# Optimization experiments

Measured on AMD Instinct MI355X. Metric: run time of the kernel, lower is better.

Reference implementation:

```python
import jax, jax.numpy as jnp
import numpy as np

B, S, D, V, H, P, L, STEPS = 8, 128, 512, 32768, 8, 2048, 4, 3
DK = D // H
SCALE = 1.0 / np.sqrt(DK)


def setup_inputs() -> dict:
    key = jax.random.key(0)
    ks = jax.random.split(key, 16)

    def n(k, shape, s=0.02):
        return jax.random.normal(k, shape, dtype=jnp.float32) * s

    return {
        'tokens': jax.random.randint(ks[0], (B, S), 0, V, dtype=jnp.int32),
        'emb': n(ks[1], (V, D)),
        'in_proj_w': n(ks[2], (L, 3 * D, D)),
        'in_proj_b': jnp.zeros((L, 3 * D), jnp.float32),
        'attn_out_w': n(ks[3], (L, D, D)),
        'attn_out_b': jnp.zeros((L, D), jnp.float32),
        'ln1_w': jnp.ones((L, D), jnp.float32),
        'ln1_b': jnp.zeros((L, D), jnp.float32),
        'lstm_wih': n(ks[4], (L, 4 * D, D)),
        'lstm_whh': n(ks[5], (L, 4 * D, D)),
        'lstm_bih': jnp.zeros((L, 4 * D), jnp.float32),
        'lstm_bhh': jnp.zeros((L, 4 * D), jnp.float32),
        'ff_w1': n(ks[6], (L, P, D)),
        'ff_b1': jnp.zeros((L, P), jnp.float32),
        'ff_w2': n(ks[7], (L, D, P)),
        'ff_b2': jnp.zeros((L, D), jnp.float32),
        'ln2_w': jnp.ones((L, D), jnp.float32),
        'ln2_b': jnp.zeros((L, D), jnp.float32),
        'head_w': n(ks[8], (V, D)),
        'head_b': jnp.zeros((V,), jnp.float32),
    }


def _layernorm(x, w, b, eps=1e-5):
    m = x.mean(-1, keepdims=True)
    v = x.var(-1, keepdims=True)
    return (x - m) * jax.lax.rsqrt(v + eps) * w + b


def _forward(tokens, emb, in_proj_w, in_proj_b, attn_out_w, attn_out_b,
             ln1_w, ln1_b, lstm_wih, lstm_whh, lstm_bih, lstm_bhh,
             ff_w1, ff_b1, ff_w2, ff_b2, ln2_w, ln2_b, head_w, head_b):
    # embedding; PositionalEncoding.forward in the source is a no-op (returns x)
    x = emb[tokens]                       # (B, S, D)
    x = x.transpose(1, 0, 2)              # seq-first (S, B, D) like nn.MultiheadAttention
    causal = jnp.triu(jnp.ones((S, S), bool), 1)  # True above diagonal -> masked

    for l in range(L):
        # --- self attention (eval mode, dropout=0) ---
        qkv = x @ in_proj_w[l].T + in_proj_b[l]        # (S, B, 3D)
        q, k, v = jnp.split(qkv, 3, axis=-1)
        def heads(t):  # (S, B, D) -> (B, H, S, DK)
            return t.reshape(S, B, H, DK).transpose(1, 2, 0, 3)
        q, k, v = heads(q), heads(k), heads(v)
        scores = jnp.einsum('bhqd,bhkd->bhqk', q, k) * SCALE
        scores = jnp.where(causal, jnp.finfo(scores.dtype).min, scores)
        w = jax.nn.softmax(scores, axis=-1)
        o = jnp.einsum('bhqk,bhkd->bhqd', w, v)        # (B, H, S, DK)
        o = o.transpose(2, 0, 1, 3).reshape(S, B, D)
        attn = o @ attn_out_w[l].T + attn_out_b[l]
        x = _layernorm(x + attn, ln1_w[l], ln1_b[l])

        # --- latent recurrence: per-token LSTM cell carried for STEPS steps ---
        residual = x
        latent = x.transpose(1, 0, 2).reshape(B * S, D)  # (B*S, D)
        h = jnp.zeros_like(latent)
        c = jnp.zeros_like(latent)
        for _ in range(STEPS):
            gates = latent @ lstm_wih[l].T + lstm_bih[l] + h @ lstm_whh[l].T + lstm_bhh[l]
            i_g, f_g, g_g, o_g = jnp.split(gates, 4, axis=-1)  # torch gate order i,f,g,o
            c = jax.nn.sigmoid(f_g) * c + jax.nn.sigmoid(i_g) * jnp.tanh(g_g)
            h = jax.nn.sigmoid(o_g) * jnp.tanh(c)
            latent = h
        latent = latent.reshape(B, S, D).transpose(1, 0, 2)  # (S, B, D)
        latent = residual + latent

        # --- feed forward ---
        ff = jax.nn.relu(latent @ ff_w1[l].T + ff_b1[l]) @ ff_w2[l].T + ff_b2[l]
        x = _layernorm(latent + ff, ln2_w[l], ln2_b[l])

    logits = x @ head_w.T + head_b        # (S, B, V)
    return logits.transpose(1, 0, 2)      # (B, S, V)


def reference(tokens, emb, in_proj_w, in_proj_b, attn_out_w, attn_out_b,
              ln1_w, ln1_b, lstm_wih, lstm_whh, lstm_bih, lstm_bhh,
              ff_w1, ff_b1, ff_w2, ff_b2, ln2_w, ln2_b, head_w, head_b):
    return _forward(tokens, emb, in_proj_w, in_proj_b, attn_out_w, attn_out_b,
                    ln1_w, ln1_b, lstm_wih, lstm_whh, lstm_bih, lstm_bhh,
                    ff_w1, ff_b1, ff_w2, ff_b2, ln2_w, ln2_b, head_w, head_b)
```

## Files before the change

kernel.cpp:

```cpp
#include <hip/hip_runtime.h>
#include <hip/hip_bf16.h>
#include <math.h>

typedef unsigned short ushort_t;
typedef __bf16 bf16x8 __attribute__((ext_vector_type(8)));
typedef float f32x4 __attribute__((ext_vector_type(4)));

constexpr int Bb = 8, Ss = 128, Dd = 512, Vv = 32768, Hh = 8, Pp = 2048, Ll = 4;
constexpr int Tt = Bb * Ss;
constexpr int DK = Dd / Hh;
constexpr float SCALE = 0.125f;

__device__ __forceinline__ ushort_t f2b(float f) {
    unsigned u = __float_as_uint(f);
    unsigned r = (u + 0x7FFFu + ((u >> 16) & 1u)) >> 16;
    return (ushort_t)r;
}

__device__ __forceinline__ void gload_lds16(const void* g, void* l) {
    __builtin_amdgcn_global_load_lds((const __attribute__((address_space(1))) void*)g,
                                     (__attribute__((address_space(3))) void*)l, 16, 0, 0);
}

struct CvtSegs {
    const float* a[8];
    const float* b[8];
    void*        d[8];
    long         end4[8];
    int          mode[8];
};

__global__ __launch_bounds__(256) void cvt_all_k(CvtSegs s) {
    long i = (long)blockIdx.x * 256 + threadIdx.x;
    int k = 0;
    while (k < 7 && i >= s.end4[k]) ++k;
    long base = k ? s.end4[k - 1] : 0;
    long j = i - base;
    int mode = s.mode[k];
    long srcj = j;
    if (mode == 2 || mode == 3) {
        const long per = 2048L * 128;
        long layer = j / per, rem = j % per;
        long drow = rem >> 7, col4 = rem & 127;
        long g = (drow >> 4) & 3, d = (drow >> 6) * 16 + (drow & 15);
        srcj = layer * per + (g * 512 + d) * 128 + col4;
    } else if (mode == 4) {
        const long per = 512;
        long layer = j / per, rem = j % per;
        long e0 = rem * 4;
        long g = (e0 >> 4) & 3, d = (e0 >> 6) * 16 + (e0 & 15);
        srcj = layer * per + (g * 512 + d) / 4;
    }
    float4 v = reinterpret_cast<const float4*>(s.a[k])[srcj];
    if (s.b[k]) {
        float4 vb = reinterpret_cast<const float4*>(s.b[k])[srcj];
        v.x += vb.x; v.y += vb.y; v.z += vb.z; v.w += vb.w;
    }
    if (mode == 4) {
        reinterpret_cast<float4*>(s.d[k])[j] = v;
    } else {
        ushort4 o;
        o.x = f2b(v.x); o.y = f2b(v.y); o.z = f2b(v.z); o.w = f2b(v.w);
        reinterpret_cast<ushort4*>(s.d[k])[j] = o;
    }
}

__global__ __launch_bounds__(128) void embed_k(const int* __restrict__ tokens,
                                               const float* __restrict__ emb,
                                               float* __restrict__ X,
                                               ushort_t* __restrict__ Xb) {
    int t = blockIdx.x;
    int tok = tokens[t];
    float4 v = reinterpret_cast<const float4*>(emb + (long)tok * Dd)[threadIdx.x];
    reinterpret_cast<float4*>(X + (long)t * Dd)[threadIdx.x] = v;
    ushort4 o;
    o.x = f2b(v.x); o.y = f2b(v.y); o.z = f2b(v.z); o.w = f2b(v.w);
    reinterpret_cast<ushort4*>(Xb + (long)t * Dd)[threadIdx.x] = o;
}

template <int BM, int BN, int BK, int EPI>
__global__ __launch_bounds__(256) void gemm_bf16(const ushort_t* __restrict__ A,
                                                 const ushort_t* __restrict__ W,
                                                 const float* __restrict__ b1,
                                                 float* __restrict__ C,
                                                 ushort_t* __restrict__ Cb,
                                                 float* __restrict__ cst,
                                                 const float* __restrict__ addsrc,
                                                 float* __restrict__ lat,
                                                 ushort_t* __restrict__ latb,
                                                 int M, int N, int K) {
    constexpr int CH = BK / 8;
    constexpr int SH = (CH == 4) ? 1 : 0;
    constexpr int WM = BM / 2, WN = BN / 2;
    constexpr int FM = WM / 16, FN = WN / 16;
    constexpr int LA = BM * BK / 2048;
    constexpr int LW = BN * BK / 2048;

    __shared__ __align__(16) ushort_t As[2][BM * BK];
    __shared__ __align__(16) ushort_t Ws[2][BN * BK];

    const int tid = threadIdx.x;
    const int lane = tid & 63, wid = tid >> 6;
    const int wr = wid >> 1, wc = wid & 1;
    const int row0 = blockIdx.y * BM, col0 = blockIdx.x * BN;

    auto stage = [&](int buf, int k0) {
#pragma unroll
        for (int i = 0; i < LA; ++i) {
            int j = i * 256 + tid;
            int prow = j / CH;
            int pkg = j & (CH - 1);
            int skg = pkg ^ ((prow >> SH) & (CH - 1));
            gload_lds16(A + (long)(row0 + prow) * K + k0 + skg * 8,
                        &As[buf][(i * 256 + wid * 64) * 8]);
        }
#pragma unroll
        for (int i = 0; i < LW; ++i) {
            int j = i * 256 + tid;
            int prow = j / CH;
            int pkg = j & (CH - 1);
            int skg = pkg ^ ((prow >> SH) & (CH - 1));
            gload_lds16(W + (long)(col0 + prow) * K + k0 + skg * 8,
                        &Ws[buf][(i * 256 + wid * 64) * 8]);
        }
    };

    f32x4 acc[FM][FN];
#pragma unroll
    for (int m = 0; m < FM; ++m)
#pragma unroll
        for (int n = 0; n < FN; ++n) acc[m][n] = (f32x4)(0.0f);

    const int NT = K / BK;
    stage(0, 0);
    __syncthreads();
    for (int t = 0; t < NT; ++t) {
        int cur = t & 1;
        if (t + 1 < NT) stage(cur ^ 1, (t + 1) * BK);
        const ushort_t* Ab = As[cur];
        const ushort_t* Wb = Ws[cur];
#pragma unroll
        for (int kk = 0; kk < BK / 32; ++kk) {
            bf16x8 af[FM], wf[FN];
#pragma unroll
            for (int m = 0; m < FM; ++m) {
                int r = wr * WM + m * 16 + (lane & 15);
                int cl = kk * 4 + (lane >> 4);
                int cs = cl ^ ((r >> SH) & (CH - 1));
                af[m] = *reinterpret_cast<const bf16x8*>(&Ab[r * BK + cs * 8]);
            }
#pragma unroll
            for (int n = 0; n < FN; ++n) {
                int r = wc * WN + n * 16 + (lane & 15);
                int cl = kk * 4 + (lane >> 4);
                int cs = cl ^ ((r >> SH) & (CH - 1));
                wf[n] = *reinterpret_cast<const bf16x8*>(&Wb[r * BK + cs * 8]);
            }
#pragma unroll
            for (int m = 0; m < FM; ++m)
#pragma unroll
                for (int n = 0; n < FN; ++n)
                    acc[m][n] = __builtin_amdgcn_mfma_f32_16x16x32_bf16(
                        af[m], wf[n], acc[m][n], 0, 0, 0);
        }
        __syncthreads();
    }

    if constexpr (EPI <= 2) {
#pragma unroll
        for (int n = 0; n < FN; ++n) {
            int col = col0 + wc * WN + n * 16 + (lane & 15);
            float bias = b1[col];
#pragma unroll
            for (int m = 0; m < FM; ++m) {
#pragma unroll
                for (int j = 0; j < 4; ++j) {
                    int row = row0 + wr * WM + m * 16 + (lane >> 4) * 4 + j;
                    float v = acc[m][n][j] + bias;
                    if (EPI == 2) v = fmaxf(v, 0.f);
                    if (EPI == 0) C[(long)row * N + col] = v;
                    else          Cb[(long)row * N + col] = f2b(v);
                }
            }
        }
    } else {
        const int L = lane & 15;
        const int d = ((col0 >> 6) + wc) * 16 + L;
        float bI = b1[col0 + wc * WN + 0 * 16 + L];
        float bF = b1[col0 + wc * WN + 1 * 16 + L];
        float bG = b1[col0 + wc * WN + 2 * 16 + L];
        float bO = b1[col0 + wc * WN + 3 * 16 + L];
#pragma unroll
        for (int m = 0; m < FM; ++m) {
#pragma unroll
            for (int j = 0; j < 4; ++j) {
                int row = row0 + wr * WM + m * 16 + (lane >> 4) * 4 + j;
                long idx = (long)row * Dd + d;
                float gi = acc[m][0][j] + bI;
                float gf = acc[m][1][j] + bF;
                float gg = acc[m][2][j] + bG;
                float go = acc[m][3][j] + bO;
                float si = 1.f / (1.f + expf(-gi));
                float sf = 1.f / (1.f + expf(-gf));
                float so = 1.f / (1.f + expf(-go));
                float cold = (EPI == 3) ? 0.f : cst[idx];
                float cn = sf * cold + si * tanhf(gg);
                float hn = so * tanhf(cn);
                if (EPI == 5) {
                    float o = addsrc[idx] + hn;
                    lat[idx] = o;
                    latb[idx] = f2b(o);
                } else {
                    cst[idx] = cn;
                    Cb[idx] = f2b(hn);
                }
            }
        }
    }
}

__global__ __launch_bounds__(256) void attn_k(const ushort_t* __restrict__ qkv,
                                              ushort_t* __restrict__ Ob) {
    const int blk = blockIdx.x;
    const int qb = blk & 1;
    const int bh = blk >> 1;
    const int h = bh & 7, b = bh >> 3;
    const int tid = threadIdx.x, lane = tid & 63, wid = tid >> 6;
    const int wr = wid >> 1, wc = wid & 1;
    const long qp = 3 * Dd;

    __shared__ __align__(16) char smem[32768];
    ushort_t* Qs = (ushort_t*)smem;
    ushort_t* Ks = (ushort_t*)(smem + 8192);
    float*    Sf = (float*)smem;
    ushort_t* Ps = (ushort_t*)smem;
    ushort_t* Vt = (ushort_t*)(smem + 16384);

#pragma unroll
    for (int i = 0; i < 2; ++i) {
        int j = i * 256 + tid;
        int r = j >> 3, cl = j & 7, cs = cl ^ (r & 7);
        bf16x8 v = *reinterpret_cast<const bf16x8*>(
            qkv + (long)(b * Ss + qb * 64 + r) * qp + h * DK + cl * 8);
        *reinterpret_cast<bf16x8*>(Qs + r * 64 + cs * 8) = v;
    }
#pragma unroll
    for (int i = 0; i < 4; ++i) {
        int j = i * 256 + tid;
        int r = j >> 3, cl = j & 7, cs = cl ^ (r & 7);
        bf16x8 v = *reinterpret_cast<const bf16x8*>(
            qkv + (long)(b * Ss + r) * qp + Dd + h * DK + cl * 8);
        *reinterpret_cast<bf16x8*>(Ks + r * 64 + cs * 8) = v;
    }
    __syncthreads();

    f32x4 acc[2][4];
#pragma unroll
    for (int m = 0; m < 2; ++m)
#pragma unroll
        for (int n = 0; n < 4; ++n) acc[m][n] = (f32x4)(0.0f);
#pragma unroll
    for (int kk = 0; kk < 2; ++kk) {
        bf16x8 af[2], wf[4];
#pragma unroll
        for (int m = 0; m < 2; ++m) {
            int r = wr * 32 + m * 16 + (lane & 15);
            int cl = kk * 4 + (lane >> 4), cs = cl ^ (r & 7);
            af[m] = *reinterpret_cast<const bf16x8*>(Qs + r * 64 + cs * 8);
        }
#pragma unroll
        for (int n = 0; n < 4; ++n) {
            int r = wc * 64 + n * 16 + (lane & 15);
            int cl = kk * 4 + (lane >> 4), cs = cl ^ (r & 7);
            wf[n] = *reinterpret_cast<const bf16x8*>(Ks + r * 64 + cs * 8);
        }
#pragma unroll
        for (int m = 0; m < 2; ++m)
#pragma unroll
            for (int n = 0; n < 4; ++n)
                acc[m][n] = __builtin_amdgcn_mfma_f32_16x16x32_bf16(
                    af[m], wf[n], acc[m][n], 0, 0, 0);
    }
    __syncthreads();
#pragma unroll
    for (int m = 0; m < 2; ++m)
#pragma unroll
        for (int n = 0; n < 4; ++n)
#pragma unroll
            for (int j = 0; j < 4; ++j) {
                int row = wr * 32 + m * 16 + (lane >> 4) * 4 + j;
                int col = wc * 64 + n * 16 + (lane & 15);
                Sf[row * 128 + col] = acc[m][n][j] * SCALE;
            }
    __syncthreads();

    const int r = tid >> 2, q4 = tid & 3;
    const int qglob = qb * 64 + r;
    const int kbase = q4 * 32;
    float pv[32];
    float mx = -INFINITY;
#pragma unroll
    for (int i4 = 0; i4 < 8; ++i4) {
        int c4 = (i4 + (r & 7)) & 7;
        float4 v = *reinterpret_cast<const float4*>(&Sf[r * 128 + kbase + c4 * 4]);
#pragma unroll
        for (int e = 0; e < 4; ++e) {
            int kcol = kbase + c4 * 4 + e;
            float s = (e == 0) ? v.x : (e == 1) ? v.y : (e == 2) ? v.z : v.w;
            pv[i4 * 4 + e] = s;
            if (kcol <= qglob) mx = fmaxf(mx, s);
        }
    }
    mx = fmaxf(mx, __shfl_xor(mx, 1));
    mx = fmaxf(mx, __shfl_xor(mx, 2));
    float sum = 0.f;
#pragma unroll
    for (int i4 = 0; i4 < 8; ++i4) {
        int c4 = (i4 + (r & 7)) & 7;
#pragma unroll
        for (int e = 0; e < 4; ++e) {
            int kcol = kbase + c4 * 4 + e;
            float p = (kcol <= qglob) ? expf(pv[i4 * 4 + e] - mx) : 0.f;
            pv[i4 * 4 + e] = p;
            sum += p;
        }
    }
    sum += __shfl_xor(sum, 1);
    sum += __shfl_xor(sum, 2);
    float inv = 1.f / sum;
    __syncthreads();

#pragma unroll
    for (int i4 = 0; i4 < 8; ++i4) {
        int c4 = (i4 + (r & 7)) & 7;
#pragma unroll
        for (int e2 = 0; e2 < 2; ++e2) {
            int k0 = kbase + c4 * 4 + e2 * 2;
            int cl = k0 >> 3, cs = cl ^ (r & 15);
            ushort2 pr;
            pr.x = f2b(pv[i4 * 4 + e2 * 2] * inv);
            pr.y = f2b(pv[i4 * 4 + e2 * 2 + 1] * inv);
            *reinterpret_cast<ushort2*>(Ps + r * 128 + cs * 8 + (k0 & 7)) = pr;
        }
    }
#pragma unroll
    for (int i = 0; i < 4; ++i) {
        int j = i * 256 + tid;
        int s = j >> 3, dc = j & 7;
        bf16x8 v = *reinterpret_cast<const bf16x8*>(
            qkv + (long)(b * Ss + s) * qp + 2 * Dd + h * DK + dc * 8);
        int cl = s >> 3;
#pragma unroll
        for (int e = 0; e < 8; ++e) {
            int d = dc * 8 + e;
            int cs = cl ^ (d & 15);
            Vt[d * 128 + cs * 8 + (s & 7)] = ((ushort_t*)&v)[e];
        }
    }
    __syncthreads();

    f32x4 acc2[2][2];
#pragma unroll
    for (int m = 0; m < 2; ++m)
#pragma unroll
        for (int n = 0; n < 2; ++n) acc2[m][n] = (f32x4)(0.0f);
#pragma unroll
    for (int kk = 0; kk < 4; ++kk) {
        bf16x8 af[2], wf[2];
#pragma unroll
        for (int m = 0; m < 2; ++m) {
            int rr = wr * 32 + m * 16 + (lane & 15);
            int cl = kk * 4 + (lane >> 4), cs = cl ^ (rr & 15);
            af[m] = *reinterpret_cast<const bf16x8*>(Ps + rr * 128 + cs * 8);
        }
#pragma unroll
        for (int n = 0; n < 2; ++n) {
            int rd = wc * 32 + n * 16 + (lane & 15);
            int cl = kk * 4 + (lane >> 4), cs = cl ^ (rd & 15);
            wf[n] = *reinterpret_cast<const bf16x8*>(Vt + rd * 128 + cs * 8);
        }
#pragma unroll
        for (int m = 0; m < 2; ++m)
#pragma unroll
            for (int n = 0; n < 2; ++n)
                acc2[m][n] = __builtin_amdgcn_mfma_f32_16x16x32_bf16(
                    af[m], wf[n], acc2[m][n], 0, 0, 0);
    }
#pragma unroll
    for (int m = 0; m < 2; ++m)
#pragma unroll
        for (int n = 0; n < 2; ++n)
#pragma unroll
            for (int j = 0; j < 4; ++j) {
                int q = wr * 32 + m * 16 + (lane >> 4) * 4 + j;
                int d = wc * 32 + n * 16 + (lane & 15);
                Ob[(long)(b * Ss + qb * 64 + q) * Dd + h * DK + d] = f2b(acc2[m][n][j]);
            }
}

__global__ __launch_bounds__(256) void add_ln_k(float* __restrict__ out,
                                                ushort_t* __restrict__ outb,
                                                const float* __restrict__ a,
                                                const float* __restrict__ bsrc,
                                                const float* __restrict__ w,
                                                const float* __restrict__ bias) {
    const int t = blockIdx.x;
    const int tid = threadIdx.x;
    float2 av = *reinterpret_cast<const float2*>(&a[(long)t * Dd + tid * 2]);
    float2 bv = *reinterpret_cast<const float2*>(&bsrc[(long)t * Dd + tid * 2]);
    float x0 = av.x + bv.x, x1 = av.y + bv.y;
    float s = x0 + x1, ss = x0 * x0 + x1 * x1;
    for (int off = 1; off < 64; off <<= 1) {
        s += __shfl_xor(s, off);
        ss += __shfl_xor(ss, off);
    }
    __shared__ float sm[4], ssm[4];
    int wid = tid >> 6;
    if ((tid & 63) == 0) { sm[wid] = s; ssm[wid] = ss; }
    __syncthreads();
    s = sm[0] + sm[1] + sm[2] + sm[3];
    ss = ssm[0] + ssm[1] + ssm[2] + ssm[3];
    float mean = s * (1.f / Dd);
    float var = ss * (1.f / Dd) - mean * mean;
    float rstd = rsqrtf(var + 1e-5f);
    float o0 = (x0 - mean) * rstd * w[tid * 2] + bias[tid * 2];
    float o1 = (x1 - mean) * rstd * w[tid * 2 + 1] + bias[tid * 2 + 1];
    out[(long)t * Dd + tid * 2]     = o0;
    out[(long)t * Dd + tid * 2 + 1] = o1;
    ushort2 ob; ob.x = f2b(o0); ob.y = f2b(o1);
    *reinterpret_cast<ushort2*>(&outb[(long)t * Dd + tid * 2]) = ob;
}

extern "C" void kernel_launch(void* const* d_in, const int* in_sizes, int n_in,
                              void* d_out, int out_size, void* d_ws, size_t ws_size,
                              hipStream_t stream) {
    const int*   tokens     = (const int*)  d_in[0];
    const float* emb        = (const float*)d_in[1];
    const float* in_proj_w  = (const float*)d_in[2];
    const float* in_proj_b  = (const float*)d_in[3];
    const float* attn_out_w = (const float*)d_in[4];
    const float* attn_out_b = (const float*)d_in[5];
    const float* ln1_w      = (const float*)d_in[6];
    const float* ln1_b      = (const float*)d_in[7];
    const float* lstm_wih   = (const float*)d_in[8];
    const float* lstm_whh   = (const float*)d_in[9];
    const float* lstm_bih   = (const float*)d_in[10];
    const float* lstm_bhh   = (const float*)d_in[11];
    const float* ff_w1      = (const float*)d_in[12];
    const float* ff_b1      = (const float*)d_in[13];
    const float* ff_w2      = (const float*)d_in[14];
    const float* ff_b2      = (const float*)d_in[15];
    const float* ln2_w      = (const float*)d_in[16];
    const float* ln2_b      = (const float*)d_in[17];
    const float* head_w     = (const float*)d_in[18];
    const float* head_bias  = (const float*)d_in[19];
    float* out = (float*)d_out;

    const long TD = (long)Tt * Dd;
    float* ws    = (float*)d_ws;
    float* X     = ws;
    float* Cst   = X + TD;
    float* LAT   = Cst + TD;
    float* Ta    = LAT + TD;
    float* Tb    = Ta + TD;
    float* biasb = Tb + TD;
    ushort_t* Xb   = (ushort_t*)(biasb + (long)Ll * 2048);
    ushort_t* H1b  = Xb + TD;
    ushort_t* H2b  = H1b + TD;
    ushort_t* LATb = H2b + TD;
    ushort_t* Tab  = LATb + TD;
    ushort_t* BIGb = Tab + TD;
    ushort_t* ipw   = BIGb + (long)Tt * 2048;
    ushort_t* aow   = ipw + (long)Ll * 3 * Dd * Dd;
    ushort_t* wihb  = aow + (long)Ll * Dd * Dd;
    ushort_t* wsumb = wihb + (long)Ll * 4 * Dd * Dd;
    ushort_t* ff1b  = wsumb + (long)Ll * 4 * Dd * Dd;
    ushort_t* ff2b  = ff1b + (long)Ll * Pp * Dd;
    ushort_t* hwb   = ff2b + (long)Ll * Dd * Pp;

    CvtSegs segs;
    long cum = 0;
    auto set = [&](int k, const float* a, const float* b, void* d, long n4, int mode) {
        segs.a[k] = a; segs.b[k] = b; segs.d[k] = d; segs.mode[k] = mode;
        cum += n4; segs.end4[k] = cum;
    };
    set(0, in_proj_w,  nullptr,  ipw,   (long)Ll * 3 * Dd * Dd / 4, 0);
    set(1, attn_out_w, nullptr,  aow,   (long)Ll * Dd * Dd / 4,     0);
    set(2, lstm_wih,   nullptr,  wihb,  (long)Ll * 4 * Dd * Dd / 4, 2);
    set(3, lstm_wih,   lstm_whh, wsumb, (long)Ll * 4 * Dd * Dd / 4, 3);
    set(4, lstm_bih,   lstm_bhh, biasb, (long)Ll * 2048 / 4,        4);
    set(5, ff_w1,      nullptr,  ff1b,  (long)Ll * Pp * Dd / 4,     0);
    set(6, ff_w2,      nullptr,  ff2b,  (long)Ll * Dd * Pp / 4,     0);
    set(7, head_w,     nullptr,  hwb,   (long)Vv * Dd / 4,          0);
    cvt_all_k<<<(int)(cum / 256), 256, 0, stream>>>(segs);

    embed_k<<<Tt, 128, 0, stream>>>(tokens, emb, X, Xb);

    for (int l = 0; l < Ll; ++l) {
        gemm_bf16<64, 128, 64, 1><<<dim3(3 * Dd / 128, Tt / 64), 256, 0, stream>>>(
            Xb, ipw + (long)l * 3 * Dd * Dd, in_proj_b + (long)l * 3 * Dd,
            nullptr, BIGb, nullptr, nullptr, nullptr, nullptr, Tt, 3 * Dd, Dd);
        attn_k<<<Bb * Hh * 2, 256, 0, stream>>>(BIGb, Tab);
        gemm_bf16<64, 64, 64, 0><<<dim3(Dd / 64, Tt / 64), 256, 0, stream>>>(
            Tab, aow + (long)l * Dd * Dd, attn_out_b + (long)l * Dd,
            Tb, nullptr, nullptr, nullptr, nullptr, nullptr, Tt, Dd, Dd);
        add_ln_k<<<Tt, 256, 0, stream>>>(X, Xb, X, Tb,
                                         ln1_w + (long)l * Dd, ln1_b + (long)l * Dd);

        const float* bl = biasb + (long)l * 2048;
        gemm_bf16<64, 128, 64, 3><<<dim3(16, 16), 256, 0, stream>>>(
            Xb, wihb + (long)l * 4 * Dd * Dd, bl,
            nullptr, H1b, Cst, nullptr, nullptr, nullptr, Tt, 4 * Dd, Dd);
        gemm_bf16<64, 128, 64, 4><<<dim3(16, 16), 256, 0, stream>>>(
            H1b, wsumb + (long)l * 4 * Dd * Dd, bl,
            nullptr, H2b, Cst, nullptr, nullptr, nullptr, Tt, 4 * Dd, Dd);
        gemm_bf16<64, 128, 64, 5><<<dim3(16, 16), 256, 0, stream>>>(
            H2b, wsumb + (long)l * 4 * Dd * Dd, bl,
            nullptr, nullptr, Cst, X, LAT, LATb, Tt, 4 * Dd, Dd);

        gemm_bf16<64, 128, 64, 2><<<dim3(Pp / 128, Tt / 64), 256, 0, stream>>>(
            LATb, ff1b + (long)l * Pp * Dd, ff_b1 + (long)l * Pp,
            nullptr, BIGb, nullptr, nullptr, nullptr, nullptr, Tt, Pp, Dd);
        gemm_bf16<64, 64, 64, 0><<<dim3(Dd / 64, Tt / 64), 256, 0, stream>>>(
            BIGb, ff2b + (long)l * Dd * Pp, ff_b2 + (long)l * Dd,
            Ta, nullptr, nullptr, nullptr, nullptr, nullptr, Tt, Dd, Pp);
        add_ln_k<<<Tt, 256, 0, stream>>>(X, Xb, LAT, Ta,
                                         ln2_w + (long)l * Dd, ln2_b + (long)l * Dd);
    }

    gemm_bf16<128, 128, 32, 0><<<dim3(Vv / 128, Tt / 128), 256, 0, stream>>>(
        Xb, hwb, head_bias,
        out, nullptr, nullptr, nullptr, nullptr, nullptr, Tt, Vv, Dd);
}
```

Measured before the change: 743.8 us.

## Triple-buffer GEMM K-loop with vmcnt waits and split-K small-N GEMMs

The GEMM mainloop moves from a double buffer with two __syncthreads per tile to a three-stage LDS ring. It prefetches two tiles ahead and uses s_waitcnt vmcnt plus a single raw s_barrier per iteration. The attention-output and FF2 GEMMs (N=512) now use split-K across blockIdx.z (2 and 4 splits) to fill more CUs, writing partial sums to separate buffers. add_ln sums those partials before the residual and layernorm. This costs more LDS per block, which may lower occupancy, and adds extra fp32 partial traffic.

```diff
diff --git a/kernel.cpp b/kernel.cpp
--- a/kernel.cpp
+++ b/kernel.cpp
@@ -10,6 +10,7 @@
 constexpr int Tt = Bb * Ss;
 constexpr int DK = Dd / Hh;
 constexpr float SCALE = 0.125f;
+constexpr long TDc = (long)Tt * Dd;
 
 __device__ __forceinline__ ushort_t f2b(float f) {
     unsigned u = __float_as_uint(f);
@@ -20,6 +21,13 @@
 __device__ __forceinline__ void gload_lds16(const void* g, void* l) {
     __builtin_amdgcn_global_load_lds((const __attribute__((address_space(1))) void*)g,
                                      (__attribute__((address_space(3))) void*)l, 16, 0, 0);
+}
+
+template <int N> __device__ __forceinline__ void vwait() {
+    asm volatile("s_waitcnt vmcnt(%0)" :: "n"(N) : "memory");
+}
+__device__ __forceinline__ void barrier_raw() {
+    asm volatile("s_barrier" ::: "memory");
 }
 
 struct CvtSegs {
@@ -78,7 +86,7 @@
     reinterpret_cast<ushort4*>(Xb + (long)t * Dd)[threadIdx.x] = o;
 }
 
-template <int BM, int BN, int BK, int EPI>
+template <int BM, int BN, int BK, int EPI, int SPLITS>
 __global__ __launch_bounds__(256) void gemm_bf16(const ushort_t* __restrict__ A,
                                                  const ushort_t* __restrict__ W,
                                                  const float* __restrict__ b1,
@@ -95,14 +103,19 @@
     constexpr int FM = WM / 16, FN = WN / 16;
     constexpr int LA = BM * BK / 2048;
     constexpr int LW = BN * BK / 2048;
-
-    __shared__ __align__(16) ushort_t As[2][BM * BK];
-    __shared__ __align__(16) ushort_t Ws[2][BN * BK];
+    constexpr int LPB = LA + LW;
+
+    __shared__ __align__(16) ushort_t As[3][BM * BK];
+    __shared__ __align__(16) ushort_t Ws[3][BN * BK];
 
     const int tid = threadIdx.x;
     const int lane = tid & 63, wid = tid >> 6;
     const int wr = wid >> 1, wc = wid & 1;
     const int row0 = blockIdx.y * BM, col0 = blockIdx.x * BN;
+    const int z = (SPLITS > 1) ? blockIdx.z : 0;
+    const int KS = K / SPLITS;
+    const int kbase = z * KS;
+    const int NT = KS / BK;
 
     auto stage = [&](int buf, int k0) {
 #pragma unroll
@@ -131,14 +144,15 @@
 #pragma unroll
         for (int n = 0; n < FN; ++n) acc[m][n] = (f32x4)(0.0f);
 
-    const int NT = K / BK;
-    stage(0, 0);
-    __syncthreads();
+    stage(0, kbase);
+    if (NT > 1) stage(1, kbase + BK);
+
     for (int t = 0; t < NT; ++t) {
-        int cur = t & 1;
-        if (t + 1 < NT) stage(cur ^ 1, (t + 1) * BK);
-        const ushort_t* Ab = As[cur];
-        const ushort_t* Wb = Ws[cur];
+        if (t + 1 < NT) vwait<LPB>(); else vwait<0>();
+        barrier_raw();
+        if (t + 2 < NT) stage((t + 2) % 3, kbase + (t + 2) * BK);
+        const ushort_t* Ab = As[t % 3];
+        const ushort_t* Wb = Ws[t % 3];
 #pragma unroll
         for (int kk = 0; kk < BK / 32; ++kk) {
             bf16x8 af[FM], wf[FN];
@@ -163,14 +177,14 @@
                     acc[m][n] = __builtin_amdgcn_mfma_f32_16x16x32_bf16(
                         af[m], wf[n], acc[m][n], 0, 0, 0);
         }
-        __syncthreads();
     }
 
     if constexpr (EPI <= 2) {
+        float* Cz = C + (long)z * M * N;
 #pragma unroll
         for (int n = 0; n < FN; ++n) {
             int col = col0 + wc * WN + n * 16 + (lane & 15);
-            float bias = b1[col];
+            float bias = (z == 0) ? b1[col] : 0.f;
 #pragma unroll
             for (int m = 0; m < FM; ++m) {
 #pragma unroll
@@ -178,7 +192,7 @@
                     int row = row0 + wr * WM + m * 16 + (lane >> 4) * 4 + j;
                     float v = acc[m][n][j] + bias;
                     if (EPI == 2) v = fmaxf(v, 0.f);
-                    if (EPI == 0) C[(long)row * N + col] = v;
+                    if (EPI == 0) Cz[(long)row * N + col] = v;
                     else          Cb[(long)row * N + col] = f2b(v);
                 }
             }
@@ -401,14 +415,19 @@
 __global__ __launch_bounds__(256) void add_ln_k(float* __restrict__ out,
                                                 ushort_t* __restrict__ outb,
                                                 const float* __restrict__ a,
-                                                const float* __restrict__ bsrc,
+                                                const float* __restrict__ parts,
+                                                int nparts,
                                                 const float* __restrict__ w,
                                                 const float* __restrict__ bias) {
     const int t = blockIdx.x;
     const int tid = threadIdx.x;
     float2 av = *reinterpret_cast<const float2*>(&a[(long)t * Dd + tid * 2]);
-    float2 bv = *reinterpret_cast<const float2*>(&bsrc[(long)t * Dd + tid * 2]);
-    float x0 = av.x + bv.x, x1 = av.y + bv.y;
+    float x0 = av.x, x1 = av.y;
+    for (int p = 0; p < nparts; ++p) {
+        float2 bv = *reinterpret_cast<const float2*>(
+            &parts[p * TDc + (long)t * Dd + tid * 2]);
+        x0 += bv.x; x1 += bv.y;
+    }
     float s = x0 + x1, ss = x0 * x0 + x1 * x1;
     for (int off = 1; off < 64; off <<= 1) {
         s += __shfl_xor(s, off);
@@ -456,14 +475,14 @@
     const float* head_bias  = (const float*)d_in[19];
     float* out = (float*)d_out;
 
-    const long TD = (long)Tt * Dd;
+    const long TD = TDc;
     float* ws    = (float*)d_ws;
     float* X     = ws;
     float* Cst   = X + TD;
     float* LAT   = Cst + TD;
     float* Ta    = LAT + TD;
-    float* Tb    = Ta + TD;
-    float* biasb = Tb + TD;
+    float* Tb    = Ta + 4 * TD;
+    float* biasb = Tb + 2 * TD;
     ushort_t* Xb   = (ushort_t*)(biasb + (long)Ll * 2048);
     ushort_t* H1b  = Xb + TD;
     ushort_t* H2b  = H1b + TD;
@@ -497,38 +516,38 @@
     embed_k<<<Tt, 128, 0, stream>>>(tokens, emb, X, Xb);
 
     for (int l = 0; l < Ll; ++l) {
-        gemm_bf16<64, 128, 64, 1><<<dim3(3 * Dd / 128, Tt / 64), 256, 0, stream>>>(
+        gemm_bf16<64, 128, 64, 1, 1><<<dim3(3 * Dd / 128, Tt / 64), 256, 0, stream>>>(
             Xb, ipw + (long)l * 3 * Dd * Dd, in_proj_b + (long)l * 3 * Dd,
             nullptr, BIGb, nullptr, nullptr, nullptr, nullptr, Tt, 3 * Dd, Dd);
         attn_k<<<Bb * Hh * 2, 256, 0, stream>>>(BIGb, Tab);
-        gemm_bf16<64, 64, 64, 0><<<dim3(Dd / 64, Tt / 64), 256, 0, stream>>>(
+        gemm_bf16<64, 64, 64, 0, 2><<<dim3(Dd / 64, Tt / 64, 2), 256, 0, stream>>>(
             Tab, aow + (long)l * Dd * Dd, attn_out_b + (long)l * Dd,
             Tb, nullptr, nullptr, nullptr, nullptr, nullptr, Tt, Dd, Dd);
-        add_ln_k<<<Tt, 256, 0, stream>>>(X, Xb, X, Tb,
+        add_ln_k<<<Tt, 256, 0, stream>>>(X, Xb, X, Tb, 2,
                                          ln1_w + (long)l * Dd, ln1_b + (long)l * Dd);
 
         const float* bl = biasb + (long)l * 2048;
-        gemm_bf16<64, 128, 64, 3><<<dim3(16, 16), 256, 0, stream>>>(
+        gemm_bf16<64, 128, 64, 3, 1><<<dim3(16, 16), 256, 0, stream>>>(
             Xb, wihb + (long)l * 4 * Dd * Dd, bl,
             nullptr, H1b, Cst, nullptr, nullptr, nullptr, Tt, 4 * Dd, Dd);
-        gemm_bf16<64, 128, 64, 4><<<dim3(16, 16), 256, 0, stream>>>(
+        gemm_bf16<64, 128, 64, 4, 1><<<dim3(16, 16), 256, 0, stream>>>(
             H1b, wsumb + (long)l * 4 * Dd * Dd, bl,
             nullptr, H2b, Cst, nullptr, nullptr, nullptr, Tt, 4 * Dd, Dd);
-        gemm_bf16<64, 128, 64, 5><<<dim3(16, 16), 256, 0, stream>>>(
+        gemm_bf16<64, 128, 64, 5, 1><<<dim3(16, 16), 256, 0, stream>>>(
             H2b, wsumb + (long)l * 4 * Dd * Dd, bl,
             nullptr, nullptr, Cst, X, LAT, LATb, Tt, 4 * Dd, Dd);
 
-        gemm_bf16<64, 128, 64, 2><<<dim3(Pp / 128, Tt / 64), 256, 0, stream>>>(
+        gemm_bf16<64, 128, 64, 2, 1><<<dim3(Pp / 128, Tt / 64), 256, 0, stream>>>(
             LATb, ff1b + (long)l * Pp * Dd, ff_b1 + (long)l * Pp,
             nullptr, BIGb, nullptr, nullptr, nullptr, nullptr, Tt, Pp, Dd);
-        gemm_bf16<64, 64, 64, 0><<<dim3(Dd / 64, Tt / 64), 256, 0, stream>>>(
+        gemm_bf16<64, 64, 64, 0, 4><<<dim3(Dd / 64, Tt / 64, 4), 256, 0, stream>>>(
             BIGb, ff2b + (long)l * Dd * Pp, ff_b2 + (long)l * Dd,
             Ta, nullptr, nullptr, nullptr, nullptr, nullptr, Tt, Dd, Pp);
-        add_ln_k<<<Tt, 256, 0, stream>>>(X, Xb, LAT, Ta,
+        add_ln_k<<<Tt, 256, 0, stream>>>(X, Xb, LAT, Ta, 4,
                                          ln2_w + (long)l * Dd, ln2_b + (long)l * Dd);
     }
 
-    gemm_bf16<128, 128, 32, 0><<<dim3(Vv / 128, Tt / 128), 256, 0, stream>>>(
+    gemm_bf16<128, 128, 32, 0, 1><<<dim3(Vv / 128, Tt / 128), 256, 0, stream>>>(
         Xb, hwb, head_bias,
         out, nullptr, nullptr, nullptr, nullptr, nullptr, Tt, Vv, Dd);
 }
```

New measurement: 686.8 us. -7.7%, faster.
